# Performance work log

Hardware: AMD Instinct MI355X
Metric: run time of the kernel (lower is better)

## Reference

```python
import jax, jax.numpy as jnp
import numpy as np

# Module hyperparameters (init_kwargs): shape_data = [n_t, n_y, n_x]
N_T, N_Y, N_X = 5, 32, 32
N = N_Y * N_X            # nb_nodes
DX = DY = DT = 1.0


def setup_inputs() -> dict:
    key = jax.random.key(0)
    k1, k2, k3 = jax.random.split(key, 3)
    n_b = 4
    kappa = jax.random.uniform(k1, (n_b, 1, N, N_T), dtype=jnp.float32)
    m = jax.random.normal(k2, (n_b, 2, N, N_T), dtype=jnp.float32)
    H = jax.random.normal(k3, (n_b, 2, 2, N, N_T), dtype=jnp.float32)
    return {"kappa": kappa, "m": m, "H": H}


def _stencil_indices():
    # 9-point stencil on the n_y x n_x grid; row-major node index = y*n_x + x.
    yy, xx = np.meshgrid(np.arange(N_Y), np.arange(N_X), indexing="ij")
    yy, xx = yy.reshape(-1), xx.reshape(-1)
    node = np.arange(N)
    offs = [(0, 0), (0, 1), (0, -1), (1, 0), (-1, 0), (1, 1), (1, -1), (-1, 1), (-1, -1)]
    rows, cols, valid = [], [], []
    for oy, ox in offs:
        ny, nx = yy + oy, xx + ox
        ok = (ny >= 0) & (ny < N_Y) & (nx >= 0) & (nx < N_X)
        rows.append(node)
        cols.append(np.where(ok, ny * N_X + nx, node))
        valid.append(ok.astype(np.float32))
    return (jnp.asarray(np.concatenate(rows)),
            jnp.asarray(np.concatenate(cols)),
            jnp.asarray(np.concatenate(valid)))

ROWS, COLS, VALID = _stencil_indices()


def _build_A(kappa, m, H):
    # Finite-difference discretization of A = kappa^2 I + m.grad - div(H grad)
    # kappa: [b,t,N]; m: [b,t,2,N]; H: [b,t,2,2,N]
    mx, my = m[..., 0, :], m[..., 1, :]
    H11, H22 = H[..., 0, 0, :], H[..., 1, 1, :]
    H12 = 0.5 * (H[..., 0, 1, :] + H[..., 1, 0, :])
    c0 = kappa ** 2 + 2.0 * H11 / DX ** 2 + 2.0 * H22 / DY ** 2   # center
    cpx = mx / (2 * DX) - H11 / DX ** 2                           # (0,+1)
    cmx = -mx / (2 * DX) - H11 / DX ** 2                          # (0,-1)
    cpy = my / (2 * DY) - H22 / DY ** 2                           # (+1,0)
    cmy = -my / (2 * DY) - H22 / DY ** 2                          # (-1,0)
    cc = H12 / (2 * DX * DY)                                      # cross term
    # order matches _stencil_indices offsets
    vals = jnp.concatenate([c0, cpx, cmx, cpy, cmy, -cc, cc, cc, -cc], axis=-1)
    vals = vals * VALID                                           # zero out-of-grid neighbors
    b, t = vals.shape[0], vals.shape[1]
    A = jnp.zeros((b, t, N, N), vals.dtype)
    return A.at[:, :, ROWS, COLS].add(vals)


def reference(kappa, m, H):
    # rearrange to [batch, time, ...] leading
    kap = jnp.transpose(kappa[:, 0], (0, 2, 1))          # [b,t,N]
    mm = jnp.transpose(m, (0, 3, 1, 2))                  # [b,t,2,N]
    HH = jnp.transpose(H, (0, 4, 1, 2, 3))               # [b,t,2,2,N]
    A = _build_A(kap, mm, HH)                            # [b,t,N,N]
    I = jnp.eye(N, dtype=A.dtype)
    M = I + DT * A                                       # M_k = Id + dt * A_k
    MM = jnp.einsum("btij,btjk->btik", M, M)             # spspmm(M_k, M_k)
    b = M.shape[0]
    Q = jnp.zeros((b, N_T * N, N_T * N), A.dtype)
    # block-tridiagonal precision matrix assembly (QR = Id)
    Q = Q.at[:, 0:N, 0:N].set(MM[:, 0])
    Q = Q.at[:, 0:N, N:2 * N].set(-M[:, 1])
    for i in range(1, N_T - 1):
        Q = Q.at[:, i * N:(i + 1) * N, (i - 1) * N:i * N].set(-M[:, i - 1])
        Q = Q.at[:, i * N:(i + 1) * N, i * N:(i + 1) * N].set(MM[:, i] + I)
        Q = Q.at[:, i * N:(i + 1) * N, (i + 1) * N:(i + 2) * N].set(-M[:, i + 1])
    i = N_T - 1
    Q = Q.at[:, i * N:(i + 1) * N, (i - 1) * N:i * N].set(-M[:, i - 1])
    Q = Q.at[:, i * N:(i + 1) * N, i * N:(i + 1) * N].set(MM[:, i])
    return Q
```

## Files before the change

### kernel.cpp

```cpp
#include <hip/hip_runtime.h>

#define NT   5
#define NY   32
#define NX   32
#define NN   1024
#define QDIM 5120
#define NB   4

typedef float vfloat4 __attribute__((ext_vector_type(4)));

__device__ const int c_oy[9] = {0, 0, 0, 1, -1, 1, 1, -1, -1};
__device__ const int c_ox[9] = {0, 1, -1, 0, 0, 1, -1, 1, -1};

__device__ __forceinline__ void stencil9(const float* __restrict__ kap,
                                         const float* __restrict__ m,
                                         const float* __restrict__ H,
                                         int b, int t, int n, float s[9]) {
    float k   = kap[((size_t)b * NN + n) * NT + t];
    float mx  = m[(((size_t)b * 2 + 0) * NN + n) * NT + t];
    float my  = m[(((size_t)b * 2 + 1) * NN + n) * NT + t];
    float H11 = H[((((size_t)b * 2 + 0) * 2 + 0) * NN + n) * NT + t];
    float H01 = H[((((size_t)b * 2 + 0) * 2 + 1) * NN + n) * NT + t];
    float H10 = H[((((size_t)b * 2 + 1) * 2 + 0) * NN + n) * NT + t];
    float H22 = H[((((size_t)b * 2 + 1) * 2 + 1) * NN + n) * NT + t];
    float cc = 0.25f * (H01 + H10);
    s[0] = 1.0f + k * k + 2.0f * H11 + 2.0f * H22;
    s[1] =  0.5f * mx - H11;
    s[2] = -0.5f * mx - H11;
    s[3] =  0.5f * my - H22;
    s[4] = -0.5f * my - H22;
    s[5] = -cc;
    s[6] =  cc;
    s[7] =  cc;
    s[8] = -cc;
    int y = n >> 5, x = n & 31;
    if (x == NX - 1) { s[1] = 0.f; s[5] = 0.f; s[7] = 0.f; }
    if (x == 0)      { s[2] = 0.f; s[6] = 0.f; s[8] = 0.f; }
    if (y == NY - 1) { s[3] = 0.f; s[5] = 0.f; s[6] = 0.f; }
    if (y == 0)      { s[4] = 0.f; s[7] = 0.f; s[8] = 0.f; }
}

__global__ __launch_bounds__(256) void spde_fused(const float* __restrict__ kap,
                                                  const float* __restrict__ m,
                                                  const float* __restrict__ H,
                                                  float* __restrict__ Q) {
    const int oy[9] = {0, 0, 0, 1, -1, 1, 1, -1, -1};
    const int ox[9] = {0, 1, -1, 0, 0, 1, -1, 1, -1};

    int row = blockIdx.x;
    int b = row / (NT * NN);
    int g = row - b * (NT * NN);
    int t = g >> 10;
    int r = g & (NN - 1);
    int ry = r >> 5, rx = r & 31;
    int tid = threadIdx.x;

    __shared__ float lds_row[3][NN];
    __shared__ float sk[9][9];
    __shared__ float moff[2][9];

    {
        vfloat4 z4 = {0.f, 0.f, 0.f, 0.f};
        vfloat4* p = (vfloat4*)&lds_row[0][0];
#pragma unroll
        for (int w = 0; w < 3; ++w) p[tid + 256 * w] = z4;
    }
    if (tid < 9) {
        int ky = ry + c_oy[tid], kx = rx + c_ox[tid];
        bool valid = ((unsigned)ky < NY) && ((unsigned)kx < NX);
        int k = valid ? (ky * NX + kx) : r;
        float s[9];
        stencil9(kap, m, H, b, t, k, s);
#pragma unroll
        for (int e = 0; e < 9; ++e)
            sk[tid][(oy[e] + 1) * 3 + (ox[e] + 1)] = s[e];
    } else if (tid == 9) {
        float s[9] = {0,0,0,0,0,0,0,0,0};
        if (t >= 1) stencil9(kap, m, H, b, t - 1, r, s);
#pragma unroll
        for (int e = 0; e < 9; ++e) moff[0][e] = -s[e];
    } else if (tid == 10) {
        float s[9] = {0,0,0,0,0,0,0,0,0};
        if (t <= NT - 2) stencil9(kap, m, H, b, t + 1, r, s);
#pragma unroll
        for (int e = 0; e < 9; ++e) moff[1][e] = -s[e];
    }
    __syncthreads();

    if (tid < 25) {
        int dy = tid / 5 - 2, dx = tid % 5 - 2;
        float a = 0.f;
#pragma unroll
        for (int d1 = 0; d1 < 9; ++d1) {
            int dy2 = dy - oy[d1], dx2 = dx - ox[d1];
            if (dy2 >= -1 && dy2 <= 1 && dx2 >= -1 && dx2 <= 1) {
                a += sk[0][(oy[d1] + 1) * 3 + (ox[d1] + 1)]
                   * sk[d1][(dy2 + 1) * 3 + (dx2 + 1)];
            }
        }
        if (tid == 12 && t >= 1 && t <= NT - 2) a += 1.0f;
        int cy = ry + dy, cx = rx + dx;
        if ((unsigned)cy < NY && (unsigned)cx < NX)
            lds_row[1][cy * NX + cx] = a;
    } else if (tid >= 32 && tid < 41) {
        if (t >= 1) {
            int d = tid - 32;
            int cy = ry + c_oy[d], cx = rx + c_ox[d];
            if ((unsigned)cy < NY && (unsigned)cx < NX)
                lds_row[0][cy * NX + cx] = moff[0][d];
        }
    } else if (tid >= 48 && tid < 57) {
        if (t <= NT - 2) {
            int d = tid - 48;
            int cy = ry + c_oy[d], cx = rx + c_ox[d];
            if ((unsigned)cy < NY && (unsigned)cx < NX)
                lds_row[2][cy * NX + cx] = moff[1][d];
        }
    }
    __syncthreads();

    float* dst = Q + ((size_t)b * QDIM + g) * QDIM + 4 * tid;
    const vfloat4* src = (const vfloat4*)&lds_row[0][4 * tid];
    vfloat4 z4 = {0.f, 0.f, 0.f, 0.f};
#pragma unroll
    for (int kk = 0; kk < NT; ++kk) {
        int z = kk - t + 1;
        vfloat4 v = ((unsigned)z < 3u) ? src[(size_t)z * (NN / 4)] : z4;
        __builtin_nontemporal_store(v, (vfloat4*)(dst + (size_t)kk * NN));
    }
}

extern "C" void kernel_launch(void* const* d_in, const int* in_sizes, int n_in,
                              void* d_out, int out_size, void* d_ws, size_t ws_size,
                              hipStream_t stream) {
    const float* kap = (const float*)d_in[0];
    const float* m   = (const float*)d_in[1];
    const float* H   = (const float*)d_in[2];
    float* Q = (float*)d_out;

    int nrows = NB * NT * NN;
    spde_fused<<<nrows, 256, 0, stream>>>(kap, m, H, Q);
}
```

Measured before the change: 413.9 us.

## Process eight output rows per block with compact banded LDS staging

Each block now handles eight consecutive Q rows instead of one. Nonzeros are staged in a compact 5-row-band LDS buffer per row rather than three full 1024-float rows. This cuts the block count eightfold and amortizes launch, zero-fill and sync overhead over more output. Each thread then writes 40 vector stores per block, which raises per-block work and LDS use, and fewer blocks are available to spread over the CUs.

```diff
diff --git a/kernel.cpp b/kernel.cpp
--- a/kernel.cpp
+++ b/kernel.cpp
@@ -6,6 +6,7 @@
 #define NN   1024
 #define QDIM 5120
 #define NB   4
+#define G    8
 
 typedef float vfloat4 __attribute__((ext_vector_type(4)));
 
@@ -40,93 +41,113 @@
     if (y == 0)      { s[4] = 0.f; s[7] = 0.f; s[8] = 0.f; }
 }
 
-__global__ __launch_bounds__(256) void spde_fused(const float* __restrict__ kap,
-                                                  const float* __restrict__ m,
-                                                  const float* __restrict__ H,
-                                                  float* __restrict__ Q) {
+__global__ __launch_bounds__(256) void spde_fused_g8(const float* __restrict__ kap,
+                                                     const float* __restrict__ m,
+                                                     const float* __restrict__ H,
+                                                     float* __restrict__ Q) {
     const int oy[9] = {0, 0, 0, 1, -1, 1, 1, -1, -1};
     const int ox[9] = {0, 1, -1, 0, 0, 1, -1, 1, -1};
 
-    int row = blockIdx.x;
-    int b = row / (NT * NN);
-    int g = row - b * (NT * NN);
-    int t = g >> 10;
-    int r = g & (NN - 1);
-    int ry = r >> 5, rx = r & 31;
+    int blk = blockIdx.x;
+    int b   = blk / (NT * (NN / G));
+    int rem = blk - b * (NT * (NN / G));
+    int t   = rem >> 7;
+    int grp = rem & 127;
+    int base = grp << 3;
+    int ry = base >> 5;
+    int rxb = base & 31;
     int tid = threadIdx.x;
 
-    __shared__ float lds_row[3][NN];
-    __shared__ float sk[9][9];
-    __shared__ float moff[2][9];
+    __shared__ float band[G * 3 * 5 * 32];
+    __shared__ float sk[G][9][9];
+    __shared__ float moff[G][2][9];
 
     {
         vfloat4 z4 = {0.f, 0.f, 0.f, 0.f};
-        vfloat4* p = (vfloat4*)&lds_row[0][0];
+        vfloat4* p = (vfloat4*)band;
 #pragma unroll
-        for (int w = 0; w < 3; ++w) p[tid + 256 * w] = z4;
+        for (int w = 0; w < 4; ++w) {
+            int idx = tid + 256 * w;
+            if (idx < (G * 3 * 5 * 32) / 4) p[idx] = z4;
+        }
     }
-    if (tid < 9) {
-        int ky = ry + c_oy[tid], kx = rx + c_ox[tid];
-        bool valid = ((unsigned)ky < NY) && ((unsigned)kx < NX);
-        int k = valid ? (ky * NX + kx) : r;
-        float s[9];
-        stencil9(kap, m, H, b, t, k, s);
+    if (tid < G * 11) {
+        int j = tid / 11, u = tid - j * 11;
+        int rj = base + j;
+        if (u < 9) {
+            int ky = ry + c_oy[u], kx = (rxb + j) + c_ox[u];
+            bool valid = ((unsigned)ky < NY) && ((unsigned)kx < NX);
+            int k = valid ? (ky * NX + kx) : rj;
+            float s[9];
+            stencil9(kap, m, H, b, t, k, s);
 #pragma unroll
-        for (int e = 0; e < 9; ++e)
-            sk[tid][(oy[e] + 1) * 3 + (ox[e] + 1)] = s[e];
-    } else if (tid == 9) {
-        float s[9] = {0,0,0,0,0,0,0,0,0};
-        if (t >= 1) stencil9(kap, m, H, b, t - 1, r, s);
+            for (int e = 0; e < 9; ++e)
+                sk[j][u][(oy[e] + 1) * 3 + (ox[e] + 1)] = s[e];
+        } else if (u == 9) {
+            float s[9] = {0, 0, 0, 0, 0, 0, 0, 0, 0};
+            if (t >= 1) stencil9(kap, m, H, b, t - 1, rj, s);
 #pragma unroll
-        for (int e = 0; e < 9; ++e) moff[0][e] = -s[e];
-    } else if (tid == 10) {
-        float s[9] = {0,0,0,0,0,0,0,0,0};
-        if (t <= NT - 2) stencil9(kap, m, H, b, t + 1, r, s);
+            for (int e = 0; e < 9; ++e) moff[j][0][e] = -s[e];
+        } else {
+            float s[9] = {0, 0, 0, 0, 0, 0, 0, 0, 0};
+            if (t <= NT - 2) stencil9(kap, m, H, b, t + 1, rj, s);
 #pragma unroll
-        for (int e = 0; e < 9; ++e) moff[1][e] = -s[e];
-    }
-    __syncthreads();
-
-    if (tid < 25) {
-        int dy = tid / 5 - 2, dx = tid % 5 - 2;
-        float a = 0.f;
-#pragma unroll
-        for (int d1 = 0; d1 < 9; ++d1) {
-            int dy2 = dy - oy[d1], dx2 = dx - ox[d1];
-            if (dy2 >= -1 && dy2 <= 1 && dx2 >= -1 && dx2 <= 1) {
-                a += sk[0][(oy[d1] + 1) * 3 + (ox[d1] + 1)]
-                   * sk[d1][(dy2 + 1) * 3 + (dx2 + 1)];
-            }
-        }
-        if (tid == 12 && t >= 1 && t <= NT - 2) a += 1.0f;
-        int cy = ry + dy, cx = rx + dx;
-        if ((unsigned)cy < NY && (unsigned)cx < NX)
-            lds_row[1][cy * NX + cx] = a;
-    } else if (tid >= 32 && tid < 41) {
-        if (t >= 1) {
-            int d = tid - 32;
-            int cy = ry + c_oy[d], cx = rx + c_ox[d];
-            if ((unsigned)cy < NY && (unsigned)cx < NX)
-                lds_row[0][cy * NX + cx] = moff[0][d];
-        }
-    } else if (tid >= 48 && tid < 57) {
-        if (t <= NT - 2) {
-            int d = tid - 48;
-            int cy = ry + c_oy[d], cx = rx + c_ox[d];
-            if ((unsigned)cy < NY && (unsigned)cx < NX)
-                lds_row[2][cy * NX + cx] = moff[1][d];
+            for (int e = 0; e < 9; ++e) moff[j][1][e] = -s[e];
         }
     }
     __syncthreads();
 
-    float* dst = Q + ((size_t)b * QDIM + g) * QDIM + 4 * tid;
-    const vfloat4* src = (const vfloat4*)&lds_row[0][4 * tid];
+    for (int it = tid; it < G * 43; it += 256) {
+        int j = it / 43, q = it - j * 43;
+        int rxj = rxb + j;
+        if (q < 25) {
+            int dy = q / 5 - 2, dx = q % 5 - 2;
+            float a = 0.f;
+#pragma unroll
+            for (int d1 = 0; d1 < 9; ++d1) {
+                int dy2 = dy - oy[d1], dx2 = dx - ox[d1];
+                if (dy2 >= -1 && dy2 <= 1 && dx2 >= -1 && dx2 <= 1) {
+                    a += sk[j][0][(oy[d1] + 1) * 3 + (ox[d1] + 1)]
+                       * sk[j][d1][(dy2 + 1) * 3 + (dx2 + 1)];
+                }
+            }
+            if (q == 12 && t >= 1 && t <= NT - 2) a += 1.0f;
+            int cy = ry + dy, cx = rxj + dx;
+            if ((unsigned)cy < NY && (unsigned)cx < NX)
+                band[((j * 3 + 1) * 5 + (dy + 2)) * 32 + cx] = a;
+        } else if (q < 34) {
+            int d = q - 25;
+            int cy = ry + c_oy[d], cx = rxj + c_ox[d];
+            if ((unsigned)cy < NY && (unsigned)cx < NX)
+                band[((j * 3 + 0) * 5 + (c_oy[d] + 2)) * 32 + cx] = moff[j][0][d];
+        } else {
+            int d = q - 34;
+            int cy = ry + c_oy[d], cx = rxj + c_ox[d];
+            if ((unsigned)cy < NY && (unsigned)cx < NX)
+                band[((j * 3 + 2) * 5 + (c_oy[d] + 2)) * 32 + cx] = moff[j][1][d];
+        }
+    }
+    __syncthreads();
+
+    int cy  = tid >> 3;
+    int cx4 = (tid & 7) * 4;
+    int br  = cy - (ry - 2);
+    bool inband = (unsigned)br < 5u;
+    int br_c = inband ? br : 0;
+    const float* bp = band + br_c * 32 + cx4;
+    float* dst = Q + ((size_t)b * QDIM + (size_t)t * NN + base) * QDIM + 4 * tid;
     vfloat4 z4 = {0.f, 0.f, 0.f, 0.f};
 #pragma unroll
-    for (int kk = 0; kk < NT; ++kk) {
-        int z = kk - t + 1;
-        vfloat4 v = ((unsigned)z < 3u) ? src[(size_t)z * (NN / 4)] : z4;
-        __builtin_nontemporal_store(v, (vfloat4*)(dst + (size_t)kk * NN));
+    for (int j = 0; j < G; ++j) {
+#pragma unroll
+        for (int kk = 0; kk < NT; ++kk) {
+            int z = kk - t + 1;
+            bool ok = ((unsigned)z < 3u) && inband;
+            int z_c = ((unsigned)z < 3u) ? z : 0;
+            vfloat4 v = ok ? *(const vfloat4*)(bp + (j * 3 + z_c) * 160) : z4;
+            __builtin_nontemporal_store(v,
+                (vfloat4*)(dst + (size_t)j * QDIM + kk * NN));
+        }
     }
 }
 
@@ -138,6 +159,6 @@
     const float* H   = (const float*)d_in[2];
     float* Q = (float*)d_out;
 
-    int nrows = NB * NT * NN;
-    spde_fused<<<nrows, 256, 0, stream>>>(kap, m, H, Q);
+    int nblocks = NB * NT * (NN / G);
+    spde_fused_g8<<<nblocks, 256, 0, stream>>>(kap, m, H, Q);
 }
```

Result: no change. 418.8 us (+1.2%).
